# Performance work log

Hardware: AMD Instinct MI355X
Metric: run time of the kernel (lower is better)

## Reference

```python
import jax, jax.numpy as jnp
import numpy as np

T, B, D, H = 64, 512, 512, 2048


def setup_inputs() -> dict:
    key = jax.random.key(0)
    ks = jax.random.split(key, 6)
    y0 = jax.random.normal(ks[0], (B, D), dtype=jnp.float32)
    # strictly increasing per-sample time grids with small dt for stability
    dt = jax.random.uniform(ks[1], (T, B), dtype=jnp.float32) * 0.01 + 0.001
    t = jnp.cumsum(dt, axis=0)
    W1 = jax.random.normal(ks[2], (D, H), dtype=jnp.float32) * (1.0 / np.sqrt(D))
    b1 = jnp.zeros((H,), dtype=jnp.float32)
    W2 = jax.random.normal(ks[3], (H, D), dtype=jnp.float32) * (1.0 / np.sqrt(H))
    b2 = jnp.zeros((D,), dtype=jnp.float32)
    return {"y0": y0, "t": t, "W1": W1, "b1": b1, "W2": W2, "b2": b2}


def reference(y0, t, W1, b1, W2, b2):
    # func(t, y): autonomous 2-layer tanh MLP (t unused, as in common NeuralODE funcs)
    def f(y):
        return jnp.tanh(y @ W1 + b1) @ W2 + b2

    def step(y, dt):  # y: [B, D], dt: [B]
        dtb = dt[:, None]
        k1 = dtb * f(y)
        k2 = dtb * f(y + k1 * 0.5)
        k3 = dtb * f(y + k2 * 0.5)
        k4 = dtb * f(y + k3)
        y_new = y + (k1 + 2.0 * k2 + 2.0 * k3 + k4) / 6.0
        return y_new, y_new

    dts = t[1:] - t[:-1]  # [T-1, B] per-sample step sizes
    _, ys = jax.lax.scan(step, y0, dts)
    return jnp.concatenate([y0[None], ys], axis=0)  # [T, B, D]
```

## Files before the change

### kernel.cpp

```cpp
#include <hip/hip_runtime.h>

#define Tn 64
#define Bn 512
#define Dn 512
#define Hn 2048

typedef __attribute__((ext_vector_type(8))) short s16x8;
typedef __attribute__((ext_vector_type(4))) float f32x4;
typedef __attribute__((ext_vector_type(4))) unsigned int u32x4;
typedef unsigned int u32;
typedef unsigned long long u64;
typedef unsigned short u16;

__device__ __forceinline__ u16 f2bf(float f) {
    u32 u = __builtin_bit_cast(u32, f);
    return (u16)((u + 0x7fffu + ((u >> 16) & 1u)) >> 16);
}
__device__ __forceinline__ float bf2f(u32 v) {
    return __builtin_bit_cast(float, v << 16);
}
__device__ __forceinline__ float tanh_fast(float x) {
    float e = __builtin_amdgcn_exp2f(x * 2.885390081777927f);
    return 1.0f - 2.0f * __builtin_amdgcn_rcpf(e + 1.0f);
}
__device__ __forceinline__ u32 agent_ld(const u32* p) {
    return __hip_atomic_load((u32*)p, __ATOMIC_RELAXED, __HIP_MEMORY_SCOPE_AGENT);
}
__device__ __forceinline__ void agent_st(u32* p, u32 v) {
    __hip_atomic_store(p, v, __ATOMIC_RELAXED, __HIP_MEMORY_SCOPE_AGENT);
}
__device__ __forceinline__ u32 get_xcc() {
    u32 x;
    asm volatile("s_getreg_b32 %0, hwreg(HW_REG_XCC_ID)" : "=s"(x));
    return x & 0xffu;
}

template<bool XL>
__device__ __forceinline__ void eld128(u32x4& d, u32 vo, const void* base) {
    if constexpr (XL)
        asm volatile("global_load_dwordx4 %0, %1, %2 sc0"
                     : "=v"(d) : "v"(vo), "s"(base) : "memory");
    else
        asm volatile("global_load_dwordx4 %0, %1, %2 sc0 sc1 nt"
                     : "=v"(d) : "v"(vo), "s"(base) : "memory");
}
template<bool XL>
__device__ __forceinline__ void eld32(u32& d, u32 vo, const void* base) {
    if constexpr (XL)
        asm volatile("global_load_dword %0, %1, %2 sc0"
                     : "=v"(d) : "v"(vo), "s"(base) : "memory");
    else
        asm volatile("global_load_dword %0, %1, %2 sc0 sc1 nt"
                     : "=v"(d) : "v"(vo), "s"(base) : "memory");
}
template<bool XL>
__device__ __forceinline__ void est64(void* pa, u64 v) {
    if constexpr (XL)
        asm volatile("global_store_dwordx2 %0, %1, off sc0" :: "v"(pa), "v"(v) : "memory");
    else
        asm volatile("global_store_dwordx2 %0, %1, off sc0 sc1" :: "v"(pa), "v"(v) : "memory");
}
template<bool XL>
__device__ __forceinline__ void est32(void* pa, u32 v) {
    if constexpr (XL)
        asm volatile("global_store_dword %0, %1, off sc0" :: "v"(pa), "v"(v) : "memory");
    else
        asm volatile("global_store_dword %0, %1, off sc0 sc1" :: "v"(pa), "v"(v) : "memory");
}

__global__ void pack_w(const float* __restrict__ W1, const float* __restrict__ W2,
                       u16* __restrict__ w1p, u16* __restrict__ w2p) {
    const int i = blockIdx.x * 256 + threadIdx.x;
    const int e = i & 7;
    const int lane = (i >> 3) & 63;
    const int krem = ((lane >> 4) << 3) + e;
    const int ncol = lane & 15;
    {
        const int kt = (i >> 9) & 15, nt = i >> 13;
        const int k = (kt << 5) + krem, n = (nt << 4) + ncol;
        w1p[i] = f2bf(W1[k * Hn + n]);
    }
    {
        const int kt = (i >> 9) & 63, nt = i >> 15;
        const int k = (kt << 5) + krem, n = (nt << 4) + ncol;
        w2p[i] = f2bf(W2[k * Dn + n]);
    }
}


template<bool XL>
__device__ __forceinline__ void stage_a(const u32* ybrC, char* ldsA, int tid) {
    u32x4 d0, d1;
    const u32 vo = (u32)(tid << 5);
    eld128<XL>(d0, vo, ybrC);
    eld128<XL>(d1, vo + 16u, ybrC);
    asm volatile("s_waitcnt vmcnt(0)" : "+v"(d0), "+v"(d1) :: "memory");
    const u32 row = (u32)(tid >> 5);
    const u32 dst = vo ^ ((row & 7u) << 4);
    *(u32x4*)(ldsA + dst) = d0;
    *(u32x4*)(ldsA + (dst ^ 16u)) = d1;
}

__device__ __forceinline__ void stage_a0(const float* y0, int c, char* ldsA, int tid) {
    const float4* yc = (const float4*)(y0 + (size_t)(c << 4) * Dn);
    #pragma unroll
    for (int it = 0; it < 4; ++it) {
        const int idx = (it << 9) + tid;
        const float4 v = yc[idx];
        const u32 row = (u32)idx >> 7;
        u64 pk = (u64)((u32)f2bf(v.x) | ((u32)f2bf(v.y) << 16)) |
                 ((u64)((u32)f2bf(v.z) | ((u32)f2bf(v.w) << 16)) << 32);
        const u32 dst = (row * 1024u + ((u32)(idx & 127) << 3)) ^ ((row & 7u) << 4);
        *(u64*)(ldsA + dst) = pk;
    }
}

__device__ __forceinline__ void gemm1(const char* ldsA, char* ldsH,
                                      const s16x8 (&w1r)[16], float bia,
                                      u32 abase, u32 aswz, int w, int l15, int kg) {
    f32x4 g1 = f32x4{bia, bia, bia, bia};
    #pragma unroll
    for (int kt = 0; kt < 16; ++kt) {
        const s16x8 a = *(const s16x8*)(ldsA + ((abase + ((u32)kt << 6)) ^ aswz));
        g1 = __builtin_amdgcn_mfma_f32_16x16x32_bf16(a, w1r[kt], g1, 0, 0, 0);
    }
    #pragma unroll
    for (int j = 0; j < 4; ++j) {
        const u32 row = (u32)((kg << 2) + j);
        const u32 bo = (row * 256u + (((u32)(w << 4) + (u32)l15) << 1)) ^ ((row & 7u) << 4);
        *(u16*)(ldsH + bo) = f2bf(tanh_fast(g1[j]));
    }
}

template<bool XL>
__device__ __forceinline__ void gemm2_store(const char* ldsH, char* kpC,
                                            const s16x8 (&w2r)[4][4],
                                            u32 hbase, u32 aswz, int w, int l15,
                                            int kg, int h) {
    f32x4 acc[4];
    #pragma unroll
    for (int c = 0; c < 4; ++c) acc[c] = f32x4{0.f, 0.f, 0.f, 0.f};
    #pragma unroll
    for (int ks2 = 0; ks2 < 4; ++ks2) {
        const s16x8 ha = *(const s16x8*)(ldsH + ((hbase + ((u32)ks2 << 6)) ^ aswz));
        #pragma unroll
        for (int c = 0; c < 4; ++c)
            acc[c] = __builtin_amdgcn_mfma_f32_16x16x32_bf16(ha, w2r[c][ks2], acc[c], 0, 0, 0);
    }
    #pragma unroll
    for (int c = 0; c < 4; ++c) {
        const int nt = (w << 2) + c;
        const int o = nt >> 1;
        const int sc2 = ((nt & 1) << 4) + l15;
        u64 pk = (u64)((u32)f2bf(acc[c][0]) | ((u32)f2bf(acc[c][1]) << 16)) |
                 ((u64)((u32)f2bf(acc[c][2]) | ((u32)f2bf(acc[c][3]) << 16)) << 32);
        void* pa = kpC + (size_t)((o << 4) + h) * 1024 + (u32)((sc2 << 5) + (kg << 3));
        est64<XL>(pa, pk);
    }
}

template<bool XL>
__device__ __forceinline__ void owner_phase(int s, float& ys, float& ks, float& dtv,
                                            int brow, const char* kpC, u32* ybrC,
                                            u32* fl1C, u32* fl2C,
                                            const float* tt, float* out, float b2c,
                                            int colg, int sc, int rm, int h, int tid) {
    if (tid < 16) {
        const u32 tg = (u32)(s + 1);
        while (agent_ld(fl1C + tid) < tg) __builtin_amdgcn_s_sleep(1);
    }
    __syncthreads();
    float sacc = 0.f;
    {
        const u32 bo = ((u32)h << 14) + (u32)((sc << 5) + ((rm >> 1) << 2));
        u32 t0,t1,t2,t3,t4,t5,t6,t7,t8,t9,ta,tb,tc,td,te,tf;
        eld32<XL>(t0, bo + (0u << 10), kpC);  eld32<XL>(t1, bo + (1u << 10), kpC);
        eld32<XL>(t2, bo + (2u << 10), kpC);  eld32<XL>(t3, bo + (3u << 10), kpC);
        eld32<XL>(t4, bo + (4u << 10), kpC);  eld32<XL>(t5, bo + (5u << 10), kpC);
        eld32<XL>(t6, bo + (6u << 10), kpC);  eld32<XL>(t7, bo + (7u << 10), kpC);
        eld32<XL>(t8, bo + (8u << 10), kpC);  eld32<XL>(t9, bo + (9u << 10), kpC);
        eld32<XL>(ta, bo + (10u << 10), kpC); eld32<XL>(tb, bo + (11u << 10), kpC);
        eld32<XL>(tc, bo + (12u << 10), kpC); eld32<XL>(td, bo + (13u << 10), kpC);
        eld32<XL>(te, bo + (14u << 10), kpC); eld32<XL>(tf, bo + (15u << 10), kpC);
        asm volatile("s_waitcnt vmcnt(0)"
                     : "+v"(t0),"+v"(t1),"+v"(t2),"+v"(t3),
                       "+v"(t4),"+v"(t5),"+v"(t6),"+v"(t7),
                       "+v"(t8),"+v"(t9),"+v"(ta),"+v"(tb),
                       "+v"(tc),"+v"(td),"+v"(te),"+v"(tf) :: "memory");
        const bool hi = (rm & 1);
#define ACC1(d) sacc += bf2f(hi ? ((d) >> 16) : ((d) & 0xffffu))
        ACC1(t0); ACC1(t1); ACC1(t2); ACC1(t3);
        ACC1(t4); ACC1(t5); ACC1(t6); ACC1(t7);
        ACC1(t8); ACC1(t9); ACC1(ta); ACC1(tb);
        ACC1(tc); ACC1(td); ACC1(te); ACC1(tf);
#undef ACC1
    }
    const int step = s >> 2, sub = s & 3;
    if (sub == 0)
        dtv = tt[(step + 1) * Bn + brow] - tt[step * Bn + brow];
    const float kk = dtv * (sacc + b2c);
    float yin;
    if (sub == 0)      { ks = kk;         yin = ys + 0.5f * kk; }
    else if (sub == 1) { ks += 2.f * kk;  yin = ys + 0.5f * kk; }
    else if (sub == 2) { ks += 2.f * kk;  yin = ys + kk; }
    else {
        ks += kk; ys += ks * (1.f / 6.f); yin = ys;
        __builtin_nontemporal_store(ys, &out[((step + 1) * Bn + brow) * Dn + colg]);
    }
    if (s < 251) {
        const u32 my = (u32)f2bf(yin);
        const u32 pu = (u32)__shfl_xor((int)my, 16, 64);
        if ((sc & 1) == 0) {
            u32* ba = ybrC + (rm << 8) + (h << 4) + (sc >> 1);
            est32<XL>(ba, my | (pu << 16));
        }
        asm volatile("s_waitcnt vmcnt(0)" ::: "memory");
        __syncthreads();
        if (tid == 0) agent_st(fl2C + h, (u32)(s + 1));
    }
}

template<bool XL>
__device__ __forceinline__ void ode_loop(
    const float* y0, const float* tt, float* out,
    char* A0, char* A1, char* H0, char* H1,
    const s16x8 (&w1r)[16], const s16x8 (&w2r)[4][4],
    float bia, float b2c, u32 abase, u32 aswz, u32 hbase,
    u32* ybr0, u32* ybr1, char* kp0, char* kp1,
    u32* fl1c0, u32* fl1c1, u32* fl2c0, u32* fl2c1,
    int c0, int c1, int brow0, int brow1, int colg,
    int tid, int w, int l15, int kg, int sc, int rm, int h,
    float ys0, float ys1) {
    float ks0 = 0.f, ks1 = 0.f, dt0 = 0.f, dt1 = 0.f;
    #pragma unroll 1
    for (int s = 0; s < 252; ++s) {
        if (s == 0) {
            stage_a0(y0, c0, A0, tid);
        } else {
            if (tid < 16) {
                while (agent_ld(fl2c0 + tid) < (u32)s) __builtin_amdgcn_s_sleep(1);
            }
            __syncthreads();
            stage_a<XL>(ybr0, A0, tid);
        }
        __syncthreads();
        gemm1(A0, H0, w1r, bia, abase, aswz, w, l15, kg);
        __syncthreads();
        gemm2_store<XL>(H0, kp0, w2r, hbase, aswz, w, l15, kg, h);
        if (s == 0) {
            stage_a0(y0, c1, A1, tid);
        } else {
            if (tid < 16) {
                while (agent_ld(fl2c1 + tid) < (u32)s) __builtin_amdgcn_s_sleep(1);
            }
            __syncthreads();
            stage_a<XL>(ybr1, A1, tid);
        }
        __syncthreads();
        if (tid == 0) agent_st(fl1c0 + h, (u32)(s + 1));
        gemm1(A1, H1, w1r, bia, abase, aswz, w, l15, kg);
        __syncthreads();
        gemm2_store<XL>(H1, kp1, w2r, hbase, aswz, w, l15, kg, h);
        asm volatile("s_waitcnt vmcnt(0)" ::: "memory");
        __syncthreads();
        if (tid == 0) agent_st(fl1c1 + h, (u32)(s + 1));
        owner_phase<XL>(s, ys0, ks0, dt0, brow0, kp0, ybr0, fl1c0, fl2c0,
                        tt, out, b2c, colg, sc, rm, h, tid);
        owner_phase<XL>(s, ys1, ks1, dt1, brow1, kp1, ybr1, fl1c1, fl2c1,
                        tt, out, b2c, colg, sc, rm, h, tid);
    }
}

__launch_bounds__(512, 2)
__global__ void ode_v9(const float* __restrict__ y0, const float* __restrict__ tt,
                       const float* __restrict__ b1, const float* __restrict__ b2,
                       const u16* __restrict__ w1p, const u16* __restrict__ w2p,
                       float* __restrict__ out, u16* __restrict__ ybuf,
                       u16* __restrict__ kpart, u32* __restrict__ flags1,
                       u32* __restrict__ flags2, u32* __restrict__ xslot,
                       u32* __restrict__ xmode) {
    __shared__ u16 lds_A0[16 * 512], lds_A1[16 * 512];
    __shared__ u16 lds_H0[16 * 128], lds_H1[16 * 128];
    __shared__ u32 smode;
    char* A0 = (char*)lds_A0; char* A1 = (char*)lds_A1;
    char* H0 = (char*)lds_H0; char* H1 = (char*)lds_H1;

    const int tid = threadIdx.x;
    const int w = tid >> 6, lane = tid & 63, l15 = lane & 15, kg = lane >> 4;
    const int p = blockIdx.x & 15, h = blockIdx.x >> 4;
    const int c0 = p << 1, c1 = c0 + 1;

    if (tid == 0) {
        agent_st(xslot + (p << 4) + h, get_xcc() + 1u);
        if (h == 0) {
            u32 ref = 0; bool same = true;
            #pragma unroll 1
            for (int i = 0; i < 16; ++i) {
                u32 v;
                while ((v = agent_ld(xslot + (p << 4) + i)) == 0u)
                    __builtin_amdgcn_s_sleep(1);
                if (i == 0) ref = v; else same = same && (v == ref);
            }
            agent_st(xmode + p, same ? 1u : 2u);
        }
        u32 m;
        while ((m = agent_ld(xmode + p)) == 0u) __builtin_amdgcn_s_sleep(1);
        smode = m;
    }

    const int sc = tid >> 4, rm = tid & 15;
    const int colg = (h << 5) + sc;
    const int brow0 = (c0 << 4) + rm, brow1 = (c1 << 4) + rm;
    const float b2c = b2[colg];
    float ys0 = y0[brow0 * Dn + colg];
    float ys1 = y0[brow1 * Dn + colg];
    __builtin_nontemporal_store(ys0, &out[brow0 * Dn + colg]);
    __builtin_nontemporal_store(ys1, &out[brow1 * Dn + colg]);

    s16x8 w1r[16];
    #pragma unroll
    for (int kt = 0; kt < 16; ++kt)
        w1r[kt] = *(const s16x8*)&w1p[((size_t)((h << 3) + w) * 16 + kt) * 512 + (lane << 3)];
    s16x8 w2r[4][4];
    #pragma unroll
    for (int cc = 0; cc < 4; ++cc)
        #pragma unroll
        for (int ks2 = 0; ks2 < 4; ++ks2)
            w2r[cc][ks2] = *(const s16x8*)&w2p[((size_t)((w << 2) + cc) * 64 + (h << 2) + ks2) * 512 + (lane << 3)];
    const float bia = b1[(h << 7) + (w << 4) + l15];

    const u32 abase = (u32)l15 * 1024u + ((u32)kg << 4);
    const u32 aswz = ((u32)(l15 & 7)) << 4;
    const u32 hbase = (u32)l15 * 256u + ((u32)kg << 4);

    u32* ybr0 = (u32*)(ybuf + (size_t)c0 * 16 * 512);
    u32* ybr1 = (u32*)(ybuf + (size_t)c1 * 16 * 512);
    char* kp0 = (char*)kpart + (size_t)c0 * (256 * 1024);
    char* kp1 = (char*)kpart + (size_t)c1 * (256 * 1024);
    u32* fl1c0 = flags1 + (c0 << 4); u32* fl1c1 = flags1 + (c1 << 4);
    u32* fl2c0 = flags2 + (c0 << 4); u32* fl2c1 = flags2 + (c1 << 4);

    __syncthreads();
    const u32 mode = smode;

    if (mode == 1u)
        ode_loop<true>(y0, tt, out, A0, A1, H0, H1, w1r, w2r, bia, b2c,
                       abase, aswz, hbase, ybr0, ybr1, kp0, kp1,
                       fl1c0, fl1c1, fl2c0, fl2c1, c0, c1, brow0, brow1, colg,
                       tid, w, l15, kg, sc, rm, h, ys0, ys1);
    else
        ode_loop<false>(y0, tt, out, A0, A1, H0, H1, w1r, w2r, bia, b2c,
                        abase, aswz, hbase, ybr0, ybr1, kp0, kp1,
                        fl1c0, fl1c1, fl2c0, fl2c1, c0, c1, brow0, brow1, colg,
                        tid, w, l15, kg, sc, rm, h, ys0, ys1);
}

__launch_bounds__(512, 2)
__global__ void ode_rk4_fb(const float* __restrict__ y0, const float* __restrict__ tt,
                           const float* __restrict__ b1, const float* __restrict__ b2,
                           const u16* __restrict__ w1p, const u16* __restrict__ w2p,
                           float* __restrict__ out) {
    __shared__ u16 lds_ys[16 * Dn];
    __shared__ u16 lds_hid[16 * Hn];
    __shared__ float lds_dt[16];
    const int tid = threadIdx.x;
    const int w = tid >> 6, lane = tid & 63, l15 = lane & 15, kgrp = lane >> 4;
    const int row0 = blockIdx.x << 4;
    float yreg[4][4], ksum[4][4], kk[4][4];
    float b1v[16], b2v[4], dtv[4];
    #pragma unroll
    for (int nt = 0; nt < 16; ++nt) b1v[nt] = b1[(w << 8) + (nt << 4) + l15];
    #pragma unroll
    for (int c = 0; c < 4; ++c) b2v[c] = b2[(w << 6) + (c << 4) + l15];
    #pragma unroll
    for (int c = 0; c < 4; ++c)
        #pragma unroll
        for (int j = 0; j < 4; ++j) {
            const int rr = (kgrp << 2) + j;
            const int col = (w << 6) + (c << 4) + l15;
            const float v = y0[(row0 + rr) * Dn + col];
            yreg[c][j] = v; ksum[c][j] = 0.f; kk[c][j] = 0.f;
            out[(row0 + rr) * Dn + col] = v;
        }
    const u16* wv1 = w1p + ((w << 4) * (16 * 512)) + (lane << 3);
    const u16* wv2 = w2p + ((w << 2) * (64 * 512)) + (lane << 3);
    const int arow = l15;
    const unsigned swzA = (unsigned)((arow & 7) << 3);
    for (int step = 0; step < Tn - 1; ++step) {
        if (tid < 16)
            lds_dt[tid] = tt[(step + 1) * Bn + row0 + tid] - tt[step * Bn + row0 + tid];
        #pragma unroll 1
        for (int s = 0; s < 4; ++s) {
            const float ci = (s == 3) ? 1.0f : ((s == 0) ? 0.0f : 0.5f);
            #pragma unroll
            for (int c = 0; c < 4; ++c)
                #pragma unroll
                for (int j = 0; j < 4; ++j) {
                    const int rr = (kgrp << 2) + j;
                    const int col = (w << 6) + (c << 4) + l15;
                    lds_ys[(unsigned)((rr << 9) + col) ^ (unsigned)((rr & 7) << 3)] =
                        f2bf(yreg[c][j] + ci * kk[c][j]);
                }
            __syncthreads();
            if (s == 0) {
                #pragma unroll
                for (int j = 0; j < 4; ++j) dtv[j] = lds_dt[(kgrp << 2) + j];
            }
            f32x4 acc[16];
            #pragma unroll
            for (int nt = 0; nt < 16; ++nt)
                #pragma unroll
                for (int j = 0; j < 4; ++j) acc[nt][j] = b1v[nt];
            #pragma unroll 2
            for (int kt = 0; kt < 16; ++kt) {
                const unsigned ia = ((unsigned)((arow << 9) + (kt << 5) + (kgrp << 3))) ^ swzA;
                const s16x8 a = *(const s16x8*)&lds_ys[ia];
                #pragma unroll
                for (int nt = 0; nt < 16; ++nt) {
                    const s16x8 bfrag = *(const s16x8*)&wv1[nt * 8192 + kt * 512];
                    acc[nt] = __builtin_amdgcn_mfma_f32_16x16x32_bf16(a, bfrag, acc[nt], 0, 0, 0);
                }
            }
            #pragma unroll
            for (int nt = 0; nt < 16; ++nt)
                #pragma unroll
                for (int j = 0; j < 4; ++j) {
                    const int rr = (kgrp << 2) + j;
                    const int col = (w << 8) + (nt << 4) + l15;
                    lds_hid[(unsigned)((rr << 11) + col) ^ (unsigned)((rr & 7) << 3)] =
                        f2bf(tanh_fast(acc[nt][j]));
                }
            __syncthreads();
            f32x4 acc2[4];
            #pragma unroll
            for (int c = 0; c < 4; ++c)
                #pragma unroll
                for (int j = 0; j < 4; ++j) acc2[c][j] = 0.f;
            #pragma unroll 2
            for (int kt = 0; kt < 64; ++kt) {
                const unsigned ia = ((unsigned)((arow << 11) + (kt << 5) + (kgrp << 3))) ^ swzA;
                const s16x8 a = *(const s16x8*)&lds_hid[ia];
                #pragma unroll
                for (int c = 0; c < 4; ++c) {
                    const s16x8 bfrag = *(const s16x8*)&wv2[c * 32768 + kt * 512];
                    acc2[c] = __builtin_amdgcn_mfma_f32_16x16x32_bf16(a, bfrag, acc2[c], 0, 0, 0);
                }
            }
            const float wq = (s == 0 || s == 3) ? 1.0f : 2.0f;
            #pragma unroll
            for (int c = 0; c < 4; ++c)
                #pragma unroll
                for (int j = 0; j < 4; ++j) {
                    const float kv = dtv[j] * (acc2[c][j] + b2v[c]);
                    kk[c][j] = kv;
                    ksum[c][j] = (s == 0) ? kv : ksum[c][j] + wq * kv;
                }
        }
        #pragma unroll
        for (int c = 0; c < 4; ++c)
            #pragma unroll
            for (int j = 0; j < 4; ++j) {
                const int rr = (kgrp << 2) + j;
                const int col = (w << 6) + (c << 4) + l15;
                yreg[c][j] += ksum[c][j] * (1.0f / 6.0f);
                out[((step + 1) * Bn + row0 + rr) * Dn + col] = yreg[c][j];
            }
    }
}

extern "C" void kernel_launch(void* const* d_in, const int* in_sizes, int n_in,
                              void* d_out, int out_size, void* d_ws, size_t ws_size,
                              hipStream_t stream) {
    const float* y0 = (const float*)d_in[0];
    const float* tt = (const float*)d_in[1];
    const float* W1 = (const float*)d_in[2];
    const float* b1 = (const float*)d_in[3];
    const float* W2 = (const float*)d_in[4];
    const float* b2 = (const float*)d_in[5];
    float* out = (float*)d_out;
    char* ws = (char*)d_ws;

    const size_t sz_fl = (size_t)64 * 1024;
    const size_t sz_x = 4096;
    const size_t sz_w = (size_t)Dn * Hn * 2;
    const size_t sz_ybuf = (size_t)32 * 16 * 512 * 2;
    const size_t sz_kpart = (size_t)32 * 16 * 16 * 1024;
    const size_t needed = 2 * sz_fl + sz_x + 2 * sz_w + sz_ybuf + sz_kpart + 4096;

    u32* flags1 = (u32*)ws;
    u32* flags2 = (u32*)(ws + sz_fl);
    u32* xslot = (u32*)(ws + 2 * sz_fl);
    u32* xmode = (u32*)(ws + 2 * sz_fl + 1024);
    u16* w1p = (u16*)(ws + 2 * sz_fl + sz_x);
    u16* w2p = (u16*)(ws + 2 * sz_fl + sz_x + sz_w);
    u16* ybuf = (u16*)(ws + 2 * sz_fl + sz_x + 2 * sz_w);
    u16* kpart = (u16*)(ws + 2 * sz_fl + sz_x + 2 * sz_w + sz_ybuf);

    if (ws_size >= needed) {
        hipMemsetAsync(ws, 0, 2 * sz_fl + sz_x, stream);
        pack_w<<<4096, 256, 0, stream>>>(W1, W2, w1p, w2p);
        void* args[] = {&y0, &tt, &b1, &b2, &w1p, &w2p, &out, &ybuf, &kpart,
                        &flags1, &flags2, &xslot, &xmode};
        hipLaunchCooperativeKernel((void*)ode_v9, dim3(256), dim3(512), args, 0, stream);
    } else {
        u16* f1 = (u16*)ws;
        u16* f2 = f1 + (size_t)Dn * Hn;
        pack_w<<<4096, 256, 0, stream>>>(W1, W2, f1, f2);
        ode_rk4_fb<<<32, 512, 0, stream>>>(y0, tt, b1, b2, f1, f2, out);
    }
}
```

Baseline: 2.107 ms.

## Merge the two half-batch flag waits and barriers into joint synchronisation points

```diff
diff --git a/kernel.cpp b/kernel.cpp
--- a/kernel.cpp
+++ b/kernel.cpp
@@ -162,14 +162,8 @@
 template<bool XL>
 __device__ __forceinline__ void owner_phase(int s, float& ys, float& ks, float& dtv,
                                             int brow, const char* kpC, u32* ybrC,
-                                            u32* fl1C, u32* fl2C,
                                             const float* tt, float* out, float b2c,
                                             int colg, int sc, int rm, int h, int tid) {
-    if (tid < 16) {
-        const u32 tg = (u32)(s + 1);
-        while (agent_ld(fl1C + tid) < tg) __builtin_amdgcn_s_sleep(1);
-    }
-    __syncthreads();
     float sacc = 0.f;
     {
         const u32 bo = ((u32)h << 14) + (u32)((sc << 5) + ((rm >> 1) << 2));
@@ -214,9 +208,6 @@
             u32* ba = ybrC + (rm << 8) + (h << 4) + (sc >> 1);
             est32<XL>(ba, my | (pu << 16));
         }
-        asm volatile("s_waitcnt vmcnt(0)" ::: "memory");
-        __syncthreads();
-        if (tid == 0) agent_st(fl2C + h, (u32)(s + 1));
     }
 }
 
@@ -236,49 +227,56 @@
     for (int s = 0; s < 252; ++s) {
         if (s == 0) {
             stage_a0(y0, c0, A0, tid);
+            stage_a0(y0, c1, A1, tid);
         } else {
-            if (tid < 16) {
-                while (agent_ld(fl2c0 + tid) < (u32)s) __builtin_amdgcn_s_sleep(1);
+            if (tid < 32) {
+                u32* f = (tid < 16) ? (fl2c0 + tid) : (fl2c1 + (tid & 15));
+                while (agent_ld(f) < (u32)s) __builtin_amdgcn_s_sleep(1);
             }
             __syncthreads();
             stage_a<XL>(ybr0, A0, tid);
+            stage_a<XL>(ybr1, A1, tid);
         }
         __syncthreads();
         gemm1(A0, H0, w1r, bia, abase, aswz, w, l15, kg);
+        gemm1(A1, H1, w1r, bia, abase, aswz, w, l15, kg);
         __syncthreads();
         gemm2_store<XL>(H0, kp0, w2r, hbase, aswz, w, l15, kg, h);
-        if (s == 0) {
-            stage_a0(y0, c1, A1, tid);
-        } else {
-            if (tid < 16) {
-                while (agent_ld(fl2c1 + tid) < (u32)s) __builtin_amdgcn_s_sleep(1);
-            }
-            __syncthreads();
-            stage_a<XL>(ybr1, A1, tid);
-        }
-        __syncthreads();
-        if (tid == 0) agent_st(fl1c0 + h, (u32)(s + 1));
-        gemm1(A1, H1, w1r, bia, abase, aswz, w, l15, kg);
-        __syncthreads();
         gemm2_store<XL>(H1, kp1, w2r, hbase, aswz, w, l15, kg, h);
         asm volatile("s_waitcnt vmcnt(0)" ::: "memory");
         __syncthreads();
-        if (tid == 0) agent_st(fl1c1 + h, (u32)(s + 1));
-        owner_phase<XL>(s, ys0, ks0, dt0, brow0, kp0, ybr0, fl1c0, fl2c0,
+        if (tid == 0) {
+            agent_st(fl1c0 + h, (u32)(s + 1));
+            agent_st(fl1c1 + h, (u32)(s + 1));
+        }
+        if (tid < 32) {
+            u32* f = (tid < 16) ? (fl1c0 + tid) : (fl1c1 + (tid & 15));
+            while (agent_ld(f) < (u32)(s + 1)) __builtin_amdgcn_s_sleep(1);
+        }
+        __syncthreads();
+        owner_phase<XL>(s, ys0, ks0, dt0, brow0, kp0, ybr0,
                         tt, out, b2c, colg, sc, rm, h, tid);
-        owner_phase<XL>(s, ys1, ks1, dt1, brow1, kp1, ybr1, fl1c1, fl2c1,
+        owner_phase<XL>(s, ys1, ks1, dt1, brow1, kp1, ybr1,
                         tt, out, b2c, colg, sc, rm, h, tid);
+        if (s < 251) {
+            asm volatile("s_waitcnt vmcnt(0)" ::: "memory");
+            __syncthreads();
+            if (tid == 0) {
+                agent_st(fl2c0 + h, (u32)(s + 1));
+                agent_st(fl2c1 + h, (u32)(s + 1));
+            }
+        }
     }
 }
 
 __launch_bounds__(512, 2)
-__global__ void ode_v9(const float* __restrict__ y0, const float* __restrict__ tt,
-                       const float* __restrict__ b1, const float* __restrict__ b2,
-                       const u16* __restrict__ w1p, const u16* __restrict__ w2p,
-                       float* __restrict__ out, u16* __restrict__ ybuf,
-                       u16* __restrict__ kpart, u32* __restrict__ flags1,
-                       u32* __restrict__ flags2, u32* __restrict__ xslot,
-                       u32* __restrict__ xmode) {
+__global__ void ode_v12(const float* __restrict__ y0, const float* __restrict__ tt,
+                        const float* __restrict__ b1, const float* __restrict__ b2,
+                        const u16* __restrict__ w1p, const u16* __restrict__ w2p,
+                        float* __restrict__ out, u16* __restrict__ ybuf,
+                        u16* __restrict__ kpart, u32* __restrict__ flags1,
+                        u32* __restrict__ flags2, u32* __restrict__ xslot,
+                        u32* __restrict__ xmode) {
     __shared__ u16 lds_A0[16 * 512], lds_A1[16 * 512];
     __shared__ u16 lds_H0[16 * 128], lds_H1[16 * 128];
     __shared__ u32 smode;
@@ -501,7 +499,7 @@
         pack_w<<<4096, 256, 0, stream>>>(W1, W2, w1p, w2p);
         void* args[] = {&y0, &tt, &b1, &b2, &w1p, &w2p, &out, &ybuf, &kpart,
                         &flags1, &flags2, &xslot, &xmode};
-        hipLaunchCooperativeKernel((void*)ode_v9, dim3(256), dim3(512), args, 0, stream);
+        hipLaunchCooperativeKernel((void*)ode_v12, dim3(256), dim3(512), args, 0, stream);
     } else {
         u16* f1 = (u16*)ws;
         u16* f2 = f1 + (size_t)Dn * Hn;
```

After: 1.859 ms, median of 2. 1.13x faster.
